# Kernel tuning notes

Hardware: AMD Instinct MI355X
Metric: run time of the kernel (lower is better)

## Reference

```python
import jax, jax.numpy as jnp
import numpy as np

B, C, CI, H, W = 8, 256, 64, 64, 64  # batch, in_channels, inter_channels, spatial


def conv1x1(x, w, b):
    # x: [B,C,H,W], w: [O,C] (1x1 kernel), b: [O]
    return jnp.einsum('bchw,oc->bohw', x, w) + b[None, :, None, None]


def setup_inputs() -> dict:
    key = jax.random.key(0)
    ks = jax.random.split(key, 9)
    s_in = 1.0 / np.sqrt(C)
    s_ci = 1.0 / np.sqrt(CI)
    return {
        'x': jax.random.normal(ks[0], (B, C, H, W), dtype=jnp.float32),
        'g_w': jax.random.uniform(ks[1], (CI, C), jnp.float32, -s_in, s_in),
        'g_b': jax.random.uniform(ks[2], (CI,), jnp.float32, -s_in, s_in),
        'theta_w': jax.random.uniform(ks[3], (CI, C), jnp.float32, -s_in, s_in),
        'theta_b': jax.random.uniform(ks[4], (CI,), jnp.float32, -s_in, s_in),
        'phi_w': jax.random.uniform(ks[5], (CI, C), jnp.float32, -s_in, s_in),
        'phi_b': jax.random.uniform(ks[6], (CI,), jnp.float32, -s_in, s_in),
        'w_w': jax.random.uniform(ks[7], (C, CI), jnp.float32, -s_ci, s_ci),
        'w_b': jax.random.uniform(ks[8], (C,), jnp.float32, -s_ci, s_ci),
    }


def reference(x, g_w, g_b, theta_w, theta_b, phi_w, phi_b, w_w, w_b):
    b, c, h, w = x.shape
    n = h * w
    # 1x1 conv projections, flattened over spatial positions -> [B, N, CI]
    g_x = conv1x1(x, g_w, g_b).reshape(b, CI, n).transpose(0, 2, 1)
    theta_x = conv1x1(x, theta_w, theta_b).reshape(b, CI, n).transpose(0, 2, 1)
    phi_x = conv1x1(x, phi_w, phi_b).reshape(b, CI, n)  # [B, CI, N]
    # Full non-scaled attention over spatial positions
    f = jnp.einsum('bnc,bcm->bnm', theta_x, phi_x)       # [B, N, N]
    f_div_c = jax.nn.softmax(f, axis=-1)
    y = jnp.einsum('bnm,bmc->bnc', f_div_c, g_x)         # [B, N, CI]
    y = y.transpose(0, 2, 1).reshape(b, CI, h, w)
    w_y = conv1x1(y, w_w, w_b)                            # [B, C, H, W]
    return w_y + x
```

## Files before the change

### kernel.cpp

```cpp
#include <hip/hip_runtime.h>
#include <hip/hip_bf16.h>

#define B_  8
#define C_  256
#define CI_ 64
#define N_  4096
#define KSPLIT 4
#define KTILES (N_ / 64 / KSPLIT)

typedef short short8  __attribute__((ext_vector_type(8)));
typedef short sh4     __attribute__((ext_vector_type(4)));
typedef float floatx4 __attribute__((ext_vector_type(4)));

#define LOG2E 1.4426950408889634f

__device__ __forceinline__ unsigned short f2bf(float f) {
    unsigned u = __builtin_bit_cast(unsigned, f);
    u += 0x7FFFu + ((u >> 16) & 1u);
    return (unsigned short)(u >> 16);
}

__device__ __forceinline__ unsigned pk2(float a, float b) {
#if __has_builtin(__builtin_amdgcn_cvt_pk_bf16_f32)
    auto r = __builtin_amdgcn_cvt_pk_bf16_f32(a, b);
    return __builtin_bit_cast(unsigned, r);
#else
    return (unsigned)f2bf(a) | ((unsigned)f2bf(b) << 16);
#endif
}

__device__ __forceinline__ floatx4 mfma32(short8 a, short8 b, floatx4 c) {
    return __builtin_amdgcn_mfma_f32_16x16x32_bf16(a, b, c, 0, 0, 0);
}
__device__ __forceinline__ floatx4 mfma16(sh4 a, sh4 b, floatx4 c) {
#if __has_builtin(__builtin_amdgcn_mfma_f32_16x16x16bf16_1k)
    return __builtin_amdgcn_mfma_f32_16x16x16bf16_1k(a, b, c, 0, 0, 0);
#else
    floatx4 d;
    asm("v_mfma_f32_16x16x16_bf16 %0, %1, %2, %3" : "=v"(d) : "v"(a), "v"(b), "v"(c));
    return d;
#endif
}

__global__ __launch_bounds__(512, 4) void proj_kernel(
    const float* __restrict__ x,
    const float* __restrict__ wg, const float* __restrict__ bg,
    const float* __restrict__ wt, const float* __restrict__ bt,
    const float* __restrict__ wp, const float* __restrict__ bp,
    unsigned short* __restrict__ gws,
    unsigned short* __restrict__ tws,
    unsigned short* __restrict__ pws)
{
    constexpr int WS = 40;
    constexpr int GS = 72;
    __shared__ __align__(16) unsigned short wsl[2][192 * WS];
    __shared__ __align__(16) unsigned short gt[64 * GS];

    const int t    = threadIdx.x;
    const int lane = t & 63;
    const int w    = t >> 6;
    const int nf   = w >> 1;
    const int oh   = w & 1;
    const int l15  = lane & 15;
    const int quad = lane >> 4;
    const int n0   = blockIdx.x * 64;
    const int b    = blockIdx.y;

    floatx4 acc[6];
#pragma unroll
    for (int i = 0; i < 6; ++i) { floatx4 z = {0.f, 0.f, 0.f, 0.f}; acc[i] = z; }

    const int nA = n0 + nf * 16 + l15;
    const float* xbase = x + (size_t)b * C_ * N_ + nA;

#pragma unroll
    for (int it = 0; it < 3; ++it) {
        int u = t + it * 512;
        int row = u >> 3, c4 = u & 7;
        const float* src = (row < 64)  ? (wg + row * C_)
                         : (row < 128) ? (wt + (row - 64) * C_)
                                       : (wp + (row - 128) * C_);
        const float sc = (row >= 64 && row < 128) ? LOG2E : 1.0f;
        float4 v = *(const float4*)(src + c4 * 4);
        uint2 uu = { pk2(v.x * sc, v.y * sc), pk2(v.z * sc, v.w * sc) };
        *(uint2*)&wsl[0][row * WS + c4 * 4] = uu;
    }
    float xv[8];
#pragma unroll
    for (int j = 0; j < 8; ++j) xv[j] = xbase[(size_t)(quad * 8 + j) * N_];
    __syncthreads();

    for (int kk = 0; kk < 8; ++kk) {
        uint4 au = { pk2(xv[0], xv[1]), pk2(xv[2], xv[3]),
                     pk2(xv[4], xv[5]), pk2(xv[6], xv[7]) };
        short8 af = __builtin_bit_cast(short8, au);

        float nx[8];
        if (kk < 7) {
#pragma unroll
            for (int j = 0; j < 8; ++j)
                nx[j] = xbase[(size_t)((kk + 1) * 32 + quad * 8 + j) * N_];
#pragma unroll
            for (int it = 0; it < 3; ++it) {
                int u = t + it * 512;
                int row = u >> 3, c4 = u & 7;
                const float* src = (row < 64)  ? (wg + row * C_)
                                 : (row < 128) ? (wt + (row - 64) * C_)
                                               : (wp + (row - 128) * C_);
                const float sc = (row >= 64 && row < 128) ? LOG2E : 1.0f;
                float4 v = *(const float4*)(src + (kk + 1) * 32 + c4 * 4);
                uint2 uu = { pk2(v.x * sc, v.y * sc), pk2(v.z * sc, v.w * sc) };
                *(uint2*)&wsl[(kk + 1) & 1][row * WS + c4 * 4] = uu;
            }
        }

#pragma unroll
        for (int oti = 0; oti < 6; ++oti) {
            const int ot = oh * 6 + oti;
            short8 bf = *(const short8*)&wsl[kk & 1][(ot * 16 + l15) * WS + quad * 8];
            acc[oti] = mfma32(af, bf, acc[oti]);
        }
        __syncthreads();
#pragma unroll
        for (int j = 0; j < 8; ++j) xv[j] = nx[j];
    }

#pragma unroll
    for (int oti = 0; oti < 6; ++oti) {
        const int ot = oh * 6 + oti;
        const int oc = ot * 16 + l15;
        const float bias = (ot < 4) ? bg[oc]
                         : (ot < 8) ? bt[oc - 64] * LOG2E
                                    : bp[oc - 128];
        if (ot < 4) {
#pragma unroll
            for (int r = 0; r < 4; ++r)
                gt[oc * GS + nf * 16 + quad * 4 + r] = f2bf(acc[oti][r] + bias);
        } else {
            unsigned short* dst = (ot < 8) ? tws : pws;
            const int ci = (ot < 8) ? (oc - 64) : (oc - 128);
#pragma unroll
            for (int r = 0; r < 4; ++r) {
                int n = n0 + nf * 16 + quad * 4 + r;
                dst[((size_t)b * N_ + n) * CI_ + ci] = f2bf(acc[oti][r] + bias);
            }
        }
    }
    __syncthreads();
    {
        int ci = t >> 3, n8 = t & 7;
        uint4 v = *(const uint4*)&gt[ci * GS + n8 * 8];
        *(uint4*)(gws + ((size_t)b * CI_ + ci) * N_ + n0 + n8 * 8) = v;
    }
}

__global__ __launch_bounds__(256, 4) void attn_kernel(
    const unsigned short* __restrict__ gws,
    const unsigned short* __restrict__ tws,
    const unsigned short* __restrict__ pws,
    float* __restrict__ Opart,
    float* __restrict__ lpart)
{
    constexpr int LDW = 72;
    __shared__ __align__(16) unsigned short Vs[2][64 * LDW];

    const int t    = threadIdx.x;
    const int lane = t & 63;
    const int w    = t >> 6;
    const int l15  = lane & 15;
    const int quad = lane >> 4;
    const int b    = blockIdx.x;
    const int q0   = blockIdx.y * 128;
    const int sp   = blockIdx.z;

    const int srow = t >> 3;
    const int sc8  = t & 7;

    const unsigned short* kslice = pws + ((size_t)b * N_ + sp * (N_ / KSPLIT)) * CI_;
    const unsigned short* vbase  =
        gws + ((size_t)b * CI_ + srow) * N_ + sp * (N_ / KSPLIT) + sc8 * 8;

    short8 qf[2][2];
#pragma unroll
    for (int qg = 0; qg < 2; ++qg) {
        const unsigned short* qrow =
            tws + ((size_t)b * N_ + q0 + w * 32 + qg * 16 + l15) * CI_;
        qf[qg][0] = *(const short8*)(qrow + quad * 8);
        qf[qg][1] = *(const short8*)(qrow + 32 + quad * 8);
    }

    {
        uint4 v0 = *(const uint4*)(vbase);
        uint4 v1 = *(const uint4*)(vbase + 32 * N_);
        *(uint4*)&Vs[0][srow * LDW + sc8 * 8]        = v0;
        *(uint4*)&Vs[0][(srow + 32) * LDW + sc8 * 8] = v1;
    }
    __syncthreads();

    sh4 ones4;
#pragma unroll
    for (int j = 0; j < 4; ++j) ones4[j] = (short)0x3F80;

    floatx4 Oacc[2][4], lacc[2];
    { floatx4 z = {0.f, 0.f, 0.f, 0.f};
      lacc[0] = z; lacc[1] = z;
#pragma unroll
      for (int qg = 0; qg < 2; ++qg)
#pragma unroll
          for (int f = 0; f < 4; ++f) Oacc[qg][f] = z; }

    for (int j = 0; j < KTILES; ++j) {
        const int p  = j & 1;
        const int jn = (j + 1) & (KTILES - 1);

        uint4 pv0 = *(const uint4*)(vbase + jn * 64);
        uint4 pv1 = *(const uint4*)(vbase + 32 * N_ + jn * 64);

        const unsigned short* kt = kslice + (size_t)j * 64 * CI_;

#pragma unroll
        for (int f = 0; f < 4; ++f) {
            short8 ka0 = *(const short8*)(kt + (f * 16 + l15) * CI_ + quad * 8);
            short8 ka1 = *(const short8*)(kt + (f * 16 + l15) * CI_ + 32 + quad * 8);

            sh4 pfr[2];
#pragma unroll
            for (int qg = 0; qg < 2; ++qg) {
                floatx4 s = {0.f, 0.f, 0.f, 0.f};
                s = mfma32(ka0, qf[qg][0], s);
                s = mfma32(ka1, qf[qg][1], s);
                uint2 uu = { pk2(__builtin_amdgcn_exp2f(s[0]),
                                 __builtin_amdgcn_exp2f(s[1])),
                             pk2(__builtin_amdgcn_exp2f(s[2]),
                                 __builtin_amdgcn_exp2f(s[3])) };
                pfr[qg] = __builtin_bit_cast(sh4, uu);
                lacc[qg] = mfma16(pfr[qg], ones4, lacc[qg]);
            }
#pragma unroll
            for (int fc = 0; fc < 4; ++fc) {
                sh4 vb = *(const sh4*)&Vs[p][(fc * 16 + l15) * LDW + f * 16 + quad * 4];
#pragma unroll
                for (int qg = 0; qg < 2; ++qg)
                    Oacc[qg][fc] = mfma16(pfr[qg], vb, Oacc[qg][fc]);
            }
        }

        *(uint4*)&Vs[1 - p][srow * LDW + sc8 * 8]        = pv0;
        *(uint4*)&Vs[1 - p][(srow + 32) * LDW + sc8 * 8] = pv1;

        __syncthreads();
    }

#pragma unroll
    for (int qg = 0; qg < 2; ++qg) {
#pragma unroll
        for (int r = 0; r < 4; ++r) {
            int row = q0 + w * 32 + qg * 16 + quad * 4 + r;
            size_t obase = ((size_t)(sp * B_ + b) * N_ + row) * CI_;
#pragma unroll
            for (int fc = 0; fc < 4; ++fc)
                Opart[obase + fc * 16 + l15] = Oacc[qg][fc][r];
            if (l15 == 0)
                lpart[(size_t)(sp * B_ + b) * N_ + row] = lacc[qg][r];
        }
    }
}

__global__ __launch_bounds__(256, 4) void out_kernel(
    const float* __restrict__ Opart,
    const float* __restrict__ lpart,
    const float* __restrict__ ww,
    const float* __restrict__ wb,
    const float* __restrict__ x,
    float* __restrict__ out)
{
    constexpr int WS = 72;
    __shared__ __align__(16) unsigned short wws[128 * WS];

    const int t    = threadIdx.x;
    const int lane = t & 63;
    const int w    = t >> 6;
    const int l15  = lane & 15;
    const int quad = lane >> 4;
    const int n0   = blockIdx.x * 64;
    const int b    = blockIdx.y;
    const int ch   = blockIdx.z;

#pragma unroll
    for (int it = 0; it < 8; ++it) {
        int u = t + it * 256;
        int row = u >> 4, c4 = u & 15;
        float4 v = *(const float4*)(ww + (ch * 128 + row) * CI_ + c4 * 4);
        uint2 uu = { pk2(v.x, v.y), pk2(v.z, v.w) };
        *(uint2*)&wws[row * WS + c4 * 4] = uu;
    }
    __syncthreads();

    floatx4 acc[8];
#pragma unroll
    for (int ot = 0; ot < 8; ++ot) { floatx4 z = {0.f, 0.f, 0.f, 0.f}; acc[ot] = z; }

    const int nB = n0 + w * 16 + l15;
    float lsum = 0.f;
#pragma unroll
    for (int sp = 0; sp < KSPLIT; ++sp)
        lsum += lpart[(size_t)(sp * B_ + b) * N_ + nB];
    const float inv = 1.f / lsum;

#pragma unroll
    for (int ks = 0; ks < 2; ++ks) {
        float ysum[8] = {0.f, 0.f, 0.f, 0.f, 0.f, 0.f, 0.f, 0.f};
#pragma unroll
        for (int sp = 0; sp < KSPLIT; ++sp) {
            const float4* o = (const float4*)(Opart +
                ((size_t)(sp * B_ + b) * N_ + nB) * CI_ + ks * 32 + quad * 8);
            float4 a0 = o[0], a1 = o[1];
            ysum[0] += a0.x; ysum[1] += a0.y; ysum[2] += a0.z; ysum[3] += a0.w;
            ysum[4] += a1.x; ysum[5] += a1.y; ysum[6] += a1.z; ysum[7] += a1.w;
        }
        uint4 bu = { pk2(ysum[0] * inv, ysum[1] * inv),
                     pk2(ysum[2] * inv, ysum[3] * inv),
                     pk2(ysum[4] * inv, ysum[5] * inv),
                     pk2(ysum[6] * inv, ysum[7] * inv) };
        short8 bfrag = __builtin_bit_cast(short8, bu);
#pragma unroll
        for (int ot = 0; ot < 8; ++ot) {
            short8 afrag = *(const short8*)&wws[(ot * 16 + l15) * WS + ks * 32 + quad * 8];
            acc[ot] = mfma32(afrag, bfrag, acc[ot]);
        }
    }

#pragma unroll
    for (int ot = 0; ot < 8; ++ot) {
#pragma unroll
        for (int r = 0; r < 4; ++r) {
            int c = ch * 128 + ot * 16 + quad * 4 + r;
            size_t idx = ((size_t)b * C_ + c) * N_ + n0 + w * 16 + l15;
            out[idx] = acc[ot][r] + wb[c] + x[idx];
        }
    }
}

extern "C" void kernel_launch(void* const* d_in, const int* in_sizes, int n_in,
                              void* d_out, int out_size, void* d_ws, size_t ws_size,
                              hipStream_t stream) {
    const float* x  = (const float*)d_in[0];
    const float* gw = (const float*)d_in[1];
    const float* gb = (const float*)d_in[2];
    const float* tw = (const float*)d_in[3];
    const float* tb = (const float*)d_in[4];
    const float* pw = (const float*)d_in[5];
    const float* pb = (const float*)d_in[6];
    const float* ww = (const float*)d_in[7];
    const float* wb = (const float*)d_in[8];
    float* out = (float*)d_out;

    char* ws = (char*)d_ws;
    unsigned short* gws   = (unsigned short*)(ws);
    unsigned short* tws   = (unsigned short*)(ws + (4  << 20));
    unsigned short* pws   = (unsigned short*)(ws + (8  << 20));
    float*          Opart = (float*)        (ws + (12 << 20));
    float*          lpart = (float*)        (ws + (44 << 20));

    proj_kernel<<<dim3(64, 8), 512, 0, stream>>>(x, gw, gb, tw, tb, pw, pb, gws, tws, pws);
    attn_kernel<<<dim3(8, 32, KSPLIT), 256, 0, stream>>>(gws, tws, pws, Opart, lpart);
    out_kernel<<<dim3(64, 8, 2), 256, 0, stream>>>(Opart, lpart, ww, wb, x, out);
}
```

Measured before the change: 194.4 us.

## Store split-K partials in bf16, vectorize output epilogue, preload x and K fragments

The per-split attention partial outputs are now written and read as bf16 rather than fp32, halving that intermediate traffic between the attention and output kernels. The output kernel stages its results through shared memory so the residual add, the x read and the out write become coalesced float4 accesses. The projection kernel loads all 64 x values per thread up front instead of double-buffering them, and the attention kernel hoists all K fragment loads for a tile ahead of the MFMA loop. These trade extra registers and some bf16 rounding of the unnormalized partial sums for fewer and wider memory accesses.

After: 187.7 us. 3.5% less time.

```diff
diff --git a/kernel.cpp b/kernel.cpp
--- a/kernel.cpp
+++ b/kernel.cpp
@@ -18,6 +18,10 @@
     unsigned u = __builtin_bit_cast(unsigned, f);
     u += 0x7FFFu + ((u >> 16) & 1u);
     return (unsigned short)(u >> 16);
+}
+__device__ __forceinline__ float bf2f(unsigned short h) {
+    unsigned u = ((unsigned)h) << 16;
+    return __builtin_bit_cast(float, u);
 }
 
 __device__ __forceinline__ unsigned pk2(float a, float b) {
@@ -73,6 +77,13 @@
     const int nA = n0 + nf * 16 + l15;
     const float* xbase = x + (size_t)b * C_ * N_ + nA;
 
+    float xv[64];
+#pragma unroll
+    for (int kk = 0; kk < 8; ++kk)
+#pragma unroll
+        for (int j = 0; j < 8; ++j)
+            xv[kk * 8 + j] = xbase[(size_t)(kk * 32 + quad * 8 + j) * N_];
+
 #pragma unroll
     for (int it = 0; it < 3; ++it) {
         int u = t + it * 512;
@@ -85,21 +96,16 @@
         uint2 uu = { pk2(v.x * sc, v.y * sc), pk2(v.z * sc, v.w * sc) };
         *(uint2*)&wsl[0][row * WS + c4 * 4] = uu;
     }
-    float xv[8];
-#pragma unroll
-    for (int j = 0; j < 8; ++j) xv[j] = xbase[(size_t)(quad * 8 + j) * N_];
     __syncthreads();
 
     for (int kk = 0; kk < 8; ++kk) {
-        uint4 au = { pk2(xv[0], xv[1]), pk2(xv[2], xv[3]),
-                     pk2(xv[4], xv[5]), pk2(xv[6], xv[7]) };
+        uint4 au = { pk2(xv[kk * 8 + 0], xv[kk * 8 + 1]),
+                     pk2(xv[kk * 8 + 2], xv[kk * 8 + 3]),
+                     pk2(xv[kk * 8 + 4], xv[kk * 8 + 5]),
+                     pk2(xv[kk * 8 + 6], xv[kk * 8 + 7]) };
         short8 af = __builtin_bit_cast(short8, au);
 
-        float nx[8];
         if (kk < 7) {
-#pragma unroll
-            for (int j = 0; j < 8; ++j)
-                nx[j] = xbase[(size_t)((kk + 1) * 32 + quad * 8 + j) * N_];
 #pragma unroll
             for (int it = 0; it < 3; ++it) {
                 int u = t + it * 512;
@@ -121,8 +127,6 @@
             acc[oti] = mfma32(af, bf, acc[oti]);
         }
         __syncthreads();
-#pragma unroll
-        for (int j = 0; j < 8; ++j) xv[j] = nx[j];
     }
 
 #pragma unroll
@@ -158,7 +162,7 @@
     const unsigned short* __restrict__ gws,
     const unsigned short* __restrict__ tws,
     const unsigned short* __restrict__ pws,
-    float* __restrict__ Opart,
+    unsigned short* __restrict__ Opart,
     float* __restrict__ lpart)
 {
     constexpr int LDW = 72;
@@ -217,18 +221,21 @@
         uint4 pv1 = *(const uint4*)(vbase + 32 * N_ + jn * 64);
 
         const unsigned short* kt = kslice + (size_t)j * 64 * CI_;
-
+        short8 ka[4][2];
 #pragma unroll
         for (int f = 0; f < 4; ++f) {
-            short8 ka0 = *(const short8*)(kt + (f * 16 + l15) * CI_ + quad * 8);
-            short8 ka1 = *(const short8*)(kt + (f * 16 + l15) * CI_ + 32 + quad * 8);
-
+            ka[f][0] = *(const short8*)(kt + (f * 16 + l15) * CI_ + quad * 8);
+            ka[f][1] = *(const short8*)(kt + (f * 16 + l15) * CI_ + 32 + quad * 8);
+        }
+
+#pragma unroll
+        for (int f = 0; f < 4; ++f) {
             sh4 pfr[2];
 #pragma unroll
             for (int qg = 0; qg < 2; ++qg) {
                 floatx4 s = {0.f, 0.f, 0.f, 0.f};
-                s = mfma32(ka0, qf[qg][0], s);
-                s = mfma32(ka1, qf[qg][1], s);
+                s = mfma32(ka[f][0], qf[qg][0], s);
+                s = mfma32(ka[f][1], qf[qg][1], s);
                 uint2 uu = { pk2(__builtin_amdgcn_exp2f(s[0]),
                                  __builtin_amdgcn_exp2f(s[1])),
                              pk2(__builtin_amdgcn_exp2f(s[2]),
@@ -259,7 +266,7 @@
             size_t obase = ((size_t)(sp * B_ + b) * N_ + row) * CI_;
 #pragma unroll
             for (int fc = 0; fc < 4; ++fc)
-                Opart[obase + fc * 16 + l15] = Oacc[qg][fc][r];
+                Opart[obase + fc * 16 + l15] = f2bf(Oacc[qg][fc][r]);
             if (l15 == 0)
                 lpart[(size_t)(sp * B_ + b) * N_ + row] = lacc[qg][r];
         }
@@ -267,7 +274,7 @@
 }
 
 __global__ __launch_bounds__(256, 4) void out_kernel(
-    const float* __restrict__ Opart,
+    const unsigned short* __restrict__ Opart,
     const float* __restrict__ lpart,
     const float* __restrict__ ww,
     const float* __restrict__ wb,
@@ -275,7 +282,10 @@
     float* __restrict__ out)
 {
     constexpr int WS = 72;
-    __shared__ __align__(16) unsigned short wws[128 * WS];
+    constexpr int TS = 66;
+    __shared__ __align__(16) char smem[128 * TS * 4];
+    unsigned short* wws = (unsigned short*)smem;
+    float*          T   = (float*)smem;
 
     const int t    = threadIdx.x;
     const int lane = t & 63;
@@ -312,11 +322,11 @@
         float ysum[8] = {0.f, 0.f, 0.f, 0.f, 0.f, 0.f, 0.f, 0.f};
 #pragma unroll
         for (int sp = 0; sp < KSPLIT; ++sp) {
-            const float4* o = (const float4*)(Opart +
+            short8 ov = *(const short8*)(Opart +
                 ((size_t)(sp * B_ + b) * N_ + nB) * CI_ + ks * 32 + quad * 8);
-            float4 a0 = o[0], a1 = o[1];
-            ysum[0] += a0.x; ysum[1] += a0.y; ysum[2] += a0.z; ysum[3] += a0.w;
-            ysum[4] += a1.x; ysum[5] += a1.y; ysum[6] += a1.z; ysum[7] += a1.w;
+#pragma unroll
+            for (int e = 0; e < 8; ++e)
+                ysum[e] += bf2f((unsigned short)ov[e]);
         }
         uint4 bu = { pk2(ysum[0] * inv, ysum[1] * inv),
                      pk2(ysum[2] * inv, ysum[3] * inv),
@@ -329,15 +339,28 @@
             acc[ot] = mfma32(afrag, bfrag, acc[ot]);
         }
     }
+    __syncthreads();
 
 #pragma unroll
     for (int ot = 0; ot < 8; ++ot) {
 #pragma unroll
         for (int r = 0; r < 4; ++r) {
-            int c = ch * 128 + ot * 16 + quad * 4 + r;
-            size_t idx = ((size_t)b * C_ + c) * N_ + n0 + w * 16 + l15;
-            out[idx] = acc[ot][r] + wb[c] + x[idx];
-        }
+            int cr = ot * 16 + quad * 4 + r;
+            T[cr * TS + w * 16 + l15] = acc[ot][r] + wb[ch * 128 + cr];
+        }
+    }
+    __syncthreads();
+
+    const int c0 = t >> 4;
+    const int nq = t & 15;
+#pragma unroll
+    for (int i = 0; i < 8; ++i) {
+        int cr = c0 + 16 * i;
+        float4 tv = *(const float4*)&T[cr * TS + nq * 4];
+        size_t idx = ((size_t)b * C_ + ch * 128 + cr) * N_ + n0 + nq * 4;
+        float4 xv = *(const float4*)(x + idx);
+        float4 ov = { tv.x + xv.x, tv.y + xv.y, tv.z + xv.z, tv.w + xv.w };
+        *(float4*)(out + idx) = ov;
     }
 }
 
@@ -359,8 +382,8 @@
     unsigned short* gws   = (unsigned short*)(ws);
     unsigned short* tws   = (unsigned short*)(ws + (4  << 20));
     unsigned short* pws   = (unsigned short*)(ws + (8  << 20));
-    float*          Opart = (float*)        (ws + (12 << 20));
-    float*          lpart = (float*)        (ws + (44 << 20));
+    unsigned short* Opart = (unsigned short*)(ws + (12 << 20));
+    float*          lpart = (float*)        (ws + (28 << 20));
 
     proj_kernel<<<dim3(64, 8), 512, 0, stream>>>(x, gw, gb, tw, tb, pw, pb, gws, tws, pws);
     attn_kernel<<<dim3(8, 32, KSPLIT), 256, 0, stream>>>(gws, tws, pws, Opart, lpart);
```
